# Kernel optimization log

Hardware: AMD Instinct MI355X
Metric: run time of the kernel (lower is better)

The kernel has to match this reference:

```python
import jax, jax.numpy as jnp
import numpy as np

STRIDE = 16
HF = WF = 160
IM_H = IM_W = STRIDE * HF  # 2560
A = 15
PRE_NMS = 3000
RPN_KEEP = 300
RPN_NMS_TH = 0.7
OBJ_TH = 0.2
MIN_SIZE = 8.0
G = 7
OUT_DIM = 10
S = 2  # bilinear samples per bin per axis
NUM_FG = 3
SCORE_TH = 0.3
RCNN_NMS_TH = 0.5
FINAL_KEEP = 100
BBOX_STD = jnp.array([0.1, 0.1, 0.2, 0.2], jnp.float32)


def gen_anchors():
    base = 16.0
    anchors = []
    for r in [0.5, 1.0, 2.0]:
        for s in [2.0, 4.0, 8.0, 16.0, 32.0]:
            size = base * s
            w = size * np.sqrt(1.0 / r)
            h = size * np.sqrt(r)
            anchors.append([-w / 2, -h / 2, w / 2, h / 2])
    return jnp.asarray(np.array(anchors, np.float32))  # [A,4]


def decode_boxes(anchors, deltas):
    d = deltas * BBOX_STD
    wa = anchors[..., 2] - anchors[..., 0] + 1.0
    ha = anchors[..., 3] - anchors[..., 1] + 1.0
    cxa = anchors[..., 0] + 0.5 * wa
    cya = anchors[..., 1] + 0.5 * ha
    cx = d[..., 0] * wa + cxa
    cy = d[..., 1] * ha + cya
    w = wa * jnp.exp(jnp.minimum(d[..., 2], 4.0))
    h = ha * jnp.exp(jnp.minimum(d[..., 3], 4.0))
    boxes = jnp.stack([cx - 0.5 * w, cy - 0.5 * h, cx + 0.5 * w, cy + 0.5 * h], -1)
    hi = jnp.array([IM_W - 1.0, IM_H - 1.0, IM_W - 1.0, IM_H - 1.0], jnp.float32)
    return jnp.clip(boxes, 0.0, hi)


def greedy_nms(boxes, scores, iou_th, keep_n):
    # scores <= 0 means pre-suppressed/invalid
    N = boxes.shape[0]
    areas = jnp.maximum(boxes[:, 2] - boxes[:, 0] + 1.0, 0.0) * jnp.maximum(boxes[:, 3] - boxes[:, 1] + 1.0, 0.0)

    def body(k, st):
        sup, keep = st
        s = jnp.where(sup, -1e30, scores)
        i = jnp.argmax(s)
        valid = s[i] > -1e29
        keep = keep.at[k].set(jnp.where(valid, i.astype(jnp.int32), N))
        bi = boxes[i]
        ix1 = jnp.maximum(bi[0], boxes[:, 0]); iy1 = jnp.maximum(bi[1], boxes[:, 1])
        ix2 = jnp.minimum(bi[2], boxes[:, 2]); iy2 = jnp.minimum(bi[3], boxes[:, 3])
        inter = jnp.maximum(ix2 - ix1 + 1.0, 0.0) * jnp.maximum(iy2 - iy1 + 1.0, 0.0)
        iou = inter / jnp.maximum(areas[i] + areas - inter, 1e-6)
        sup2 = (sup | (iou > iou_th)).at[i].set(True)
        sup = jnp.where(valid, sup2, sup)
        return sup, keep

    sup0 = scores <= 0.0
    keep0 = jnp.full((keep_n,), N, jnp.int32)
    _, keep = jax.lax.fori_loop(0, keep_n, body, (sup0, keep0))
    return keep, keep < N


def rpn_proposal(rpn_cls, rpn_bbox):
    fg = rpn_cls[0, A:]                                           # [A,HF,WF] objectness
    deltas = rpn_bbox[0].reshape(A, 4, HF, WF).transpose(0, 2, 3, 1)  # [A,HF,WF,4]
    anchors = gen_anchors()
    sx = jnp.arange(WF, dtype=jnp.float32) * STRIDE
    sy = jnp.arange(HF, dtype=jnp.float32) * STRIDE
    gx, gy = jnp.meshgrid(sx, sy)                                 # [HF,WF]
    shift = jnp.stack([gx, gy, gx, gy], -1)                       # [HF,WF,4]
    all_anchors = anchors[:, None, None, :] + shift[None]         # [A,HF,WF,4]
    boxes = decode_boxes(all_anchors, deltas).reshape(-1, 4)      # [A*HF*WF,4]
    scores = fg.reshape(-1)
    w = boxes[:, 2] - boxes[:, 0] + 1.0
    h = boxes[:, 3] - boxes[:, 1] + 1.0
    ok = (w >= MIN_SIZE) & (h >= MIN_SIZE) & (scores > OBJ_TH)
    scores = jnp.where(ok, scores, 0.0)
    sc, idx = jax.lax.top_k(scores, PRE_NMS)
    bx = boxes[idx]
    keep, valid = greedy_nms(bx, sc, RPN_NMS_TH, RPN_KEEP)
    bxp = jnp.concatenate([bx, jnp.zeros((1, 4), bx.dtype)], 0)
    rois = bxp[keep] * valid[:, None].astype(bx.dtype)            # [RPN_KEEP,4]
    return rois, valid


def psroi_align(ft, rois, valid):
    # ft [490,HF,WF]; position-sensitive channel = (c*G+ph)*G+pw
    x1 = rois[:, 0] / STRIDE; y1 = rois[:, 1] / STRIDE
    x2 = rois[:, 2] / STRIDE; y2 = rois[:, 3] / STRIDE
    bw = jnp.maximum(x2 - x1, 0.1) / G
    bh = jnp.maximum(y2 - y1, 0.1) / G
    frac = (jnp.arange(S, dtype=jnp.float32) + 0.5) / S           # [S]
    grid = jnp.arange(G, dtype=jnp.float32)[None, :, None] + frac[None, None, :]  # [1,G,S]
    ys = jnp.clip(y1[:, None, None] + grid * bh[:, None, None], 0.0, HF - 1.0)    # [R,G,S]
    xs = jnp.clip(x1[:, None, None] + grid * bw[:, None, None], 0.0, WF - 1.0)
    y0 = jnp.floor(ys); x0 = jnp.floor(xs)
    wy = ys - y0; wx = xs - x0
    y0i = y0.astype(jnp.int32); x0i = x0.astype(jnp.int32)
    y1i = jnp.minimum(y0i + 1, HF - 1); x1i = jnp.minimum(x0i + 1, WF - 1)
    chan = (jnp.arange(OUT_DIM)[:, None, None] * G + jnp.arange(G)[None, :, None]) * G + jnp.arange(G)[None, None, :]
    ch = chan[None, :, :, :, None, None]                          # [1,C,G,G,1,1]
    Y0 = y0i[:, None, :, None, :, None]; Y1 = y1i[:, None, :, None, :, None]
    X0 = x0i[:, None, None, :, None, :]; X1 = x1i[:, None, None, :, None, :]
    WY = wy[:, None, :, None, :, None]; WX = wx[:, None, None, :, None, :]
    v00 = ft[ch, Y0, X0]; v01 = ft[ch, Y0, X1]
    v10 = ft[ch, Y1, X0]; v11 = ft[ch, Y1, X1]                    # [R,C,G,G,S,S]
    val = v00 * (1 - WY) * (1 - WX) + v01 * (1 - WY) * WX + v10 * WY * (1 - WX) + v11 * WY * WX
    pooled = val.mean(axis=(4, 5))                                # [R,C,G,G]
    return pooled * valid[:, None, None, None].astype(pooled.dtype)


def rcnn_proposal(cls_sm, bbox_pred, rois, valid):
    R = rois.shape[0]
    deltas = bbox_pred.reshape(R, 4, 4)[:, 1:, :]                 # [R,3,4] fg classes
    boxes = decode_boxes(rois[:, None, :], deltas)                # [R,3,4]
    scores = cls_sm[:, 1:] * valid[:, None].astype(cls_sm.dtype)  # [R,3]
    scores = jnp.where(scores > SCORE_TH, scores, 0.0)
    fb = boxes.reshape(-1, 4)
    fs = scores.reshape(-1)
    labels = jnp.tile(jnp.arange(1, NUM_FG + 1, dtype=jnp.float32), (R,))
    keep, kv = greedy_nms(fb, fs, RCNN_NMS_TH, FINAL_KEEP)
    fbp = jnp.concatenate([fb, jnp.zeros((1, 4), fb.dtype)], 0)
    fsp = jnp.concatenate([fs, jnp.zeros((1,), fs.dtype)], 0)
    flp = jnp.concatenate([labels, jnp.zeros((1,), labels.dtype)], 0)
    out = jnp.concatenate([fbp[keep], fsp[keep][:, None], flp[keep][:, None]], -1)  # [FINAL_KEEP,6]
    return out * kv[:, None].astype(out.dtype)


def setup_inputs() -> dict:
    key = jax.random.key(0)
    ks = jax.random.split(key, 9)
    return {
        'rpn_cls_prob_reshape': jax.random.uniform(ks[0], (1, 2 * A, HF, WF), jnp.float32),
        'rpn_bbox_pred': jax.random.normal(ks[1], (1, 4 * A, HF, WF), jnp.float32),
        'ft_add_left_right': jax.random.normal(ks[2], (1, OUT_DIM * G * G, HF, WF), jnp.float32),
        'w1': jax.random.normal(ks[3], (490, 2048), jnp.float32) * 0.02,
        'b1': jnp.zeros((2048,), jnp.float32),
        'w_cls': jax.random.normal(ks[4], (2048, 4), jnp.float32) * 0.02,
        'b_cls': jnp.zeros((4,), jnp.float32),
        'w_bbox': jax.random.normal(ks[5], (2048, 16), jnp.float32) * 0.02,
        'b_bbox': jnp.zeros((16,), jnp.float32),
    }


def reference(rpn_cls_prob_reshape, rpn_bbox_pred, ft_add_left_right, w1, b1, w_cls, b_cls, w_bbox, b_bbox):
    rois, valid = rpn_proposal(rpn_cls_prob_reshape, rpn_bbox_pred)
    pooled = psroi_align(ft_add_left_right[0], rois, valid)       # [R,10,7,7]
    feats = pooled.reshape(-1, OUT_DIM * G * G)                   # [R,490]
    h = jax.nn.relu(feats @ w1 + b1)
    cls_sm = jax.nn.softmax(h @ w_cls + b_cls, axis=-1)
    bbox = h @ w_bbox + b_bbox
    return rcnn_proposal(cls_sm, bbox, rois, valid)
```

## Files before the change

kernel.cpp:

```cpp
#include <hip/hip_runtime.h>
#include <stdint.h>

#define HF_ 160
#define WF_ 160
#define HFW 25600
#define A_N 15
#define NTOT 384000
#define PRE_N 3000
#define KEEP_N 300
#define FEAT_N 490
#define HID_N 2048
#define RC_N 900
#define FIN_N 100
#define TIE_CAP 1024
#define NW 47
#define NSTAGE 320
#define RNW 15
#define FC1_MT 10
#define FC1_KP 496
#define ZN (65536 * 2 + 32)

__constant__ float c_hw[15] = {
  22.627416997969522f, 45.254833995939045f, 90.509667991878090f, 181.01933598375618f, 362.03867196751236f,
  16.0f, 32.0f, 64.0f, 128.0f, 256.0f,
  11.313708498984761f, 22.627416997969522f, 45.254833995939045f, 90.509667991878090f, 181.01933598375618f
};
__constant__ float c_hh[15] = {
  11.313708498984761f, 22.627416997969522f, 45.254833995939045f, 90.509667991878090f, 181.01933598375618f,
  16.0f, 32.0f, 64.0f, 128.0f, 256.0f,
  22.627416997969522f, 45.254833995939045f, 90.509667991878090f, 181.01933598375618f, 362.03867196751236f
};

__device__ __forceinline__ void decode_one(
    float ax1, float ay1, float ax2, float ay2,
    float dx, float dy, float dw, float dh,
    float& ox1, float& oy1, float& ox2, float& oy2)
{
#pragma clang fp contract(off)
  float wa = (ax2 - ax1) + 1.0f;
  float ha = (ay2 - ay1) + 1.0f;
  float cxa = ax1 + 0.5f * wa;
  float cya = ay1 + 0.5f * ha;
  float d0 = dx * 0.1f;
  float d1 = dy * 0.1f;
  float d2 = dw * 0.2f;
  float d3 = dh * 0.2f;
  float cx = d0 * wa + cxa;
  float cy = d1 * ha + cya;
  float w  = wa * expf(fminf(d2, 4.0f));
  float h  = ha * expf(fminf(d3, 4.0f));
  float x1 = cx - 0.5f * w;
  float y1 = cy - 0.5f * h;
  float x2 = cx + 0.5f * w;
  float y2 = cy + 0.5f * h;
  ox1 = fminf(fmaxf(x1, 0.0f), 2559.0f);
  oy1 = fminf(fmaxf(y1, 0.0f), 2559.0f);
  ox2 = fminf(fmaxf(x2, 0.0f), 2559.0f);
  oy2 = fminf(fmaxf(y2, 0.0f), 2559.0f);
}

__device__ __forceinline__ float iou_ref(
    float ax1, float ay1, float ax2, float ay2, float areaA,
    float bx1, float by1, float bx2, float by2)
{
#pragma clang fp contract(off)
  float ix1 = fmaxf(ax1, bx1);
  float iy1 = fmaxf(ay1, by1);
  float ix2 = fminf(ax2, bx2);
  float iy2 = fminf(ay2, by2);
  float iw = fmaxf((ix2 - ix1) + 1.0f, 0.0f);
  float ih = fmaxf((iy2 - iy1) + 1.0f, 0.0f);
  float inter = iw * ih;
  float areaB = fmaxf((bx2 - bx1) + 1.0f, 0.0f) * fmaxf((by2 - by1) + 1.0f, 0.0f);
  float den = fmaxf(areaA + areaB - inter, 1e-6f);
  return inter / den;
}

__global__ void k_decode_score(const float* __restrict__ cls,
                               const float* __restrict__ bbox,
                               float* __restrict__ scores,
                               uint32_t* __restrict__ histzero)
{
  int e = blockIdx.x * 256 + threadIdx.x;
  if (e < ZN) histzero[e] = 0u;
  if (e >= NTOT) return;
  int a   = e / HFW;
  int rem = e - a * HFW;
  int i   = rem / WF_;
  int j   = rem - i * WF_;
  float score = cls[(A_N + a) * HFW + rem];
  float gx = (float)(j * 16);
  float gy = (float)(i * 16);
  float hw = c_hw[a], hh = c_hh[a];
  float dx = bbox[(a * 4 + 0) * HFW + rem];
  float dy = bbox[(a * 4 + 1) * HFW + rem];
  float dw = bbox[(a * 4 + 2) * HFW + rem];
  float dh = bbox[(a * 4 + 3) * HFW + rem];
  float x1, y1, x2, y2;
  decode_one(gx - hw, gy - hh, gx + hw, gy + hh, dx, dy, dw, dh, x1, y1, x2, y2);
  float bw, bh;
  {
#pragma clang fp contract(off)
    bw = (x2 - x1) + 1.0f;
    bh = (y2 - y1) + 1.0f;
  }
  bool ok = (bw >= 8.0f) && (bh >= 8.0f) && (score > 0.2f);
  scores[e] = ok ? score : 0.0f;
}

__global__ void k_hist_hi(const float* __restrict__ scores, uint32_t* __restrict__ hist)
{
  __shared__ uint32_t lh[512];
  int t = threadIdx.x;
  for (int i = t; i < 512; i += 256) lh[i] = 0u;
  __syncthreads();
  int e = blockIdx.x * 256 + t;
  if (e < NTOT) {
    float s = scores[e];
    if (s > 0.0f) {
      uint32_t b = __float_as_uint(s) >> 16;
      if (b >= 0x3E00u && b < 0x4000u) atomicAdd(&lh[b - 0x3E00u], 1u);
      else atomicAdd(&hist[b], 1u);
    }
  }
  __syncthreads();
  for (int i = t; i < 512; i += 256) {
    uint32_t v = lh[i];
    if (v) atomicAdd(&hist[0x3E00u + i], v);
  }
}

__global__ void __launch_bounds__(1024) k_findbin1(const uint32_t* __restrict__ hist,
                                                   uint32_t* __restrict__ meta)
{
  __shared__ uint32_t sfx[1024];
  __shared__ int s_chunk;
  __shared__ uint32_t s_exc;
  int t = threadIdx.x;
  if (t == 0) s_chunk = -1;
  const uint32_t* hp = hist + t * 64;
  uint32_t s = 0;
#pragma unroll
  for (int b = 0; b < 64; b++) s += hp[b];
  sfx[t] = s;
  __syncthreads();
  for (int d = 1; d < 1024; d <<= 1) {
    uint32_t v = (t + d < 1024) ? sfx[t + d] : 0u;
    __syncthreads();
    sfx[t] += v;
    __syncthreads();
  }
  uint32_t inc = sfx[t];
  uint32_t exc = (t < 1023) ? sfx[t + 1] : 0u;
  if (exc < (uint32_t)PRE_N && inc >= (uint32_t)PRE_N) { s_chunk = t; s_exc = exc; }
  __syncthreads();
  int c = s_chunk;
  if (c < 0) {
    if (t == 0) { meta[0] = 0u; meta[1] = 0u; meta[2] = 1u; }
    return;
  }
  if (t < 64) {
    uint32_t h = hist[c * 64 + t];
    uint32_t v = h;
#pragma unroll
    for (int d = 1; d < 64; d <<= 1) {
      uint32_t o = (uint32_t)__shfl_down((int)v, d);
      v += (t + d < 64) ? o : 0u;
    }
    uint32_t before = s_exc + (v - h);
    if (before < (uint32_t)PRE_N && before + h >= (uint32_t)PRE_N) {
      meta[0] = (uint32_t)(c * 64 + t);
      meta[1] = (uint32_t)PRE_N - before;
      meta[2] = 0u;
    }
  }
}

__global__ void k_hist_lo(const float* __restrict__ scores,
                          const uint32_t* __restrict__ meta,
                          uint32_t* __restrict__ hist2)
{
  if (meta[2]) return;
  uint32_t B1 = meta[0];
  int e = blockIdx.x * 256 + threadIdx.x;
  if (e >= NTOT) return;
  float s = scores[e];
  if (s <= 0.0f) return;
  uint32_t bits = __float_as_uint(s);
  if ((bits >> 16) == B1) atomicAdd(&hist2[bits & 0xFFFFu], 1u);
}

__global__ void __launch_bounds__(1024) k_findT(const uint32_t* __restrict__ hist2,
                                                uint32_t* __restrict__ meta)
{
  if (meta[2]) { if (threadIdx.x == 0) meta[3] = 0u; return; }
  __shared__ uint32_t sfx[1024];
  __shared__ int s_chunk;
  __shared__ uint32_t s_exc;
  int t = threadIdx.x;
  if (t == 0) s_chunk = -1;
  uint32_t K = meta[1];
  const uint32_t* hp = hist2 + t * 64;
  uint32_t s = 0;
#pragma unroll
  for (int b = 0; b < 64; b++) s += hp[b];
  sfx[t] = s;
  __syncthreads();
  for (int d = 1; d < 1024; d <<= 1) {
    uint32_t v = (t + d < 1024) ? sfx[t + d] : 0u;
    __syncthreads();
    sfx[t] += v;
    __syncthreads();
  }
  uint32_t inc = sfx[t];
  uint32_t exc = (t < 1023) ? sfx[t + 1] : 0u;
  if (exc < K && inc >= K) { s_chunk = t; s_exc = exc; }
  __syncthreads();
  int c = s_chunk;
  if (c < 0) { if (t == 0) meta[3] = 0u; return; }
  if (t < 64) {
    uint32_t h = hist2[c * 64 + t];
    uint32_t v = h;
#pragma unroll
    for (int d = 1; d < 64; d <<= 1) {
      uint32_t o = (uint32_t)__shfl_down((int)v, d);
      v += (t + d < 64) ? o : 0u;
    }
    uint32_t before = s_exc + (v - h);
    if (before < K && before + h >= K)
      meta[3] = (meta[0] << 16) | (uint32_t)(c * 64 + t);
  }
}

__global__ void k_compact(const float* __restrict__ scores,
                          const uint32_t* __restrict__ meta,
                          uint64_t* __restrict__ gt,
                          uint64_t* __restrict__ tie,
                          uint32_t* __restrict__ cnts)
{
  int e = blockIdx.x * 256 + threadIdx.x;
  if (e >= NTOT) return;
  float s = scores[e];
  if (s <= 0.0f) return;
  uint32_t bits = __float_as_uint(s);
  uint32_t T = meta[3];
  uint64_t key = ((uint64_t)bits << 32) | (uint32_t)(~(uint32_t)e);
  if (bits > T) {
    uint32_t p = atomicAdd(&cnts[0], 1u);
    if (p < (uint32_t)PRE_N) gt[p] = key;
  } else if (bits == T) {
    uint32_t p = atomicAdd(&cnts[1], 1u);
    if (p < (uint32_t)TIE_CAP) tie[p] = key;
  }
}

__global__ void __launch_bounds__(1024) k_sort_gather(
    const uint64_t* __restrict__ gt,
    const uint64_t* __restrict__ tie,
    const uint32_t* __restrict__ cnts,
    const float* __restrict__ bbox,
    float* __restrict__ bxx1, float* __restrict__ bxy1,
    float* __restrict__ bxx2, float* __restrict__ bxy2)
{
  __shared__ uint64_t key[4096];
  int t = threadIdx.x;
  uint32_t ngt = min(cnts[0], (uint32_t)PRE_N);
  uint32_t nte = min(cnts[1], (uint32_t)TIE_CAP);
  for (int s = t; s < 4096; s += 1024) {
    uint64_t k = 0;
    if ((uint32_t)s < ngt) k = gt[s];
    else if ((uint32_t)s < ngt + nte) k = tie[s - ngt];
    key[s] = k;
  }
  for (unsigned size = 2; size <= 4096; size <<= 1) {
    for (unsigned stride = size >> 1; stride > 0; stride >>= 1) {
      __syncthreads();
      for (unsigned i = t; i < 4096; i += 1024) {
        unsigned p = i ^ stride;
        if (p > i) {
          bool desc = ((i & size) == 0);
          uint64_t a = key[i], b = key[p];
          if (desc ? (a < b) : (a > b)) { key[i] = b; key[p] = a; }
        }
      }
    }
  }
  __syncthreads();
  for (int s = t; s < PRE_N; s += 1024) {
    uint64_t k = key[s];
    int idx = (int)(~(uint32_t)(k & 0xFFFFFFFFull));
    float x1 = 0.f, y1 = 0.f, x2 = 0.f, y2 = 0.f;
    if (idx >= 0) {
      int a   = idx / HFW;
      int rem = idx - a * HFW;
      int i   = rem / WF_;
      int j   = rem - i * WF_;
      float gx = (float)(j * 16);
      float gy = (float)(i * 16);
      float hw = c_hw[a], hh = c_hh[a];
      float dx = bbox[(a * 4 + 0) * HFW + rem];
      float dy = bbox[(a * 4 + 1) * HFW + rem];
      float dw = bbox[(a * 4 + 2) * HFW + rem];
      float dh = bbox[(a * 4 + 3) * HFW + rem];
      decode_one(gx - hw, gy - hh, gx + hw, gy + hh, dx, dy, dw, dh, x1, y1, x2, y2);
    }
    bxx1[s] = x1; bxy1[s] = y1; bxx2[s] = x2; bxy2[s] = y2;
  }
}

__global__ void __launch_bounds__(256) k_iou_mask(
    const float* __restrict__ bxx1, const float* __restrict__ bxy1,
    const float* __restrict__ bxx2, const float* __restrict__ bxy2,
    uint64_t* __restrict__ rowmask, uint64_t* __restrict__ diag)
{
  __shared__ float s1[PRE_N], s2[PRE_N], s3[PRE_N], s4[PRE_N];
  int t = threadIdx.x;
  for (int e = t; e < PRE_N; e += 256) {
    s1[e] = bxx1[e]; s2[e] = bxy1[e]; s3[e] = bxx2[e]; s4[e] = bxy2[e];
  }
  __syncthreads();
  int task = blockIdx.x * 256 + t;
  if (task >= PRE_N * NW) return;
  int row = task / NW;
  int w   = task - row * NW;
  if ((w + 1) * 64 <= row) {
    rowmask[(size_t)row * NW + w] = 0;
    return;
  }
  float ax1 = s1[row], ay1 = s2[row], ax2 = s3[row], ay2 = s4[row];
  float areaA;
  {
#pragma clang fp contract(off)
    areaA = fmaxf((ax2 - ax1) + 1.0f, 0.0f) * fmaxf((ay2 - ay1) + 1.0f, 0.0f);
  }
  int j0 = w << 6;
  uint64_t bits = 0;
  for (int off = 0; off < 64; off++) {
    int jj = (off + t) & 63;
    int j = j0 + jj;
    if (j < PRE_N) {
      float iou = iou_ref(ax1, ay1, ax2, ay2, areaA, s1[j], s2[j], s3[j], s4[j]);
      if (iou > 0.7f) bits |= 1ull << jj;
    }
  }
  rowmask[(size_t)row * NW + w] = bits;
  if (w == (row >> 6)) diag[row] = bits;
}

__global__ void __launch_bounds__(256) k_rpn_scan(
    const float* __restrict__ bxx1, const float* __restrict__ bxy1,
    const float* __restrict__ bxx2, const float* __restrict__ bxy2,
    const uint32_t* __restrict__ cnts,
    const uint64_t* __restrict__ rowmask,
    const uint64_t* __restrict__ diag,
    float* __restrict__ rois, uint32_t* __restrict__ valid)
{
  __shared__ uint64_t rowstage[NSTAGE * NW];
  __shared__ uint64_t sdiag[PRE_N];
  __shared__ int keepIdx[KEEP_N];
  __shared__ int s_nkeep;
  int t = threadIdx.x;
  for (int e = t; e < NSTAGE * NW; e += 256) rowstage[e] = rowmask[e];
  for (int e = t; e < PRE_N; e += 256) sdiag[e] = diag[e];
  __syncthreads();
  if (t < 64) {
    int lane = t;
    uint32_t Mp = min(cnts[0] + min(cnts[1], (uint32_t)TIE_CAP), (uint32_t)PRE_N);
    uint64_t sup = 0, pend = 0;
    int nk = 0;
    int nwords = (int)((Mp + 63u) >> 6);
    for (int w = 0; w < nwords && nk < KEEP_N; w++) {
      sup |= pend; pend = 0;
      uint64_t cw = (uint64_t)__shfl((unsigned long long)sup, w);
      int lim = (int)Mp - (w << 6);
      uint64_t range = (lim >= 64) ? ~0ull : ((1ull << lim) - 1ull);
      uint64_t rem = (~cw) & range;
      while (rem && nk < KEEP_N) {
        int b = __builtin_ctzll(rem);
        int i = (w << 6) + b;
        if (lane == 0) keepIdx[nk] = i;
        nk++;
        uint64_t roww = sdiag[i];
        uint64_t rowl = 0;
        if (lane < NW)
          rowl = (i < NSTAGE) ? rowstage[i * NW + lane]
                              : rowmask[(size_t)i * NW + lane];
        sup |= pend;
        pend = rowl;
        rem &= ~(roww | (1ull << b));
      }
    }
    sup |= pend;
    if (lane == 0) s_nkeep = nk;
  }
  __syncthreads();
  int nk2 = s_nkeep;
  for (int k = t; k < nk2; k += 256) {
    int i = keepIdx[k];
    rois[k * 4 + 0] = bxx1[i];
    rois[k * 4 + 1] = bxy1[i];
    rois[k * 4 + 2] = bxx2[i];
    rois[k * 4 + 3] = bxy2[i];
    valid[k] = 1u;
  }
  for (int e = nk2 * 4 + t; e < KEEP_N * 4; e += 256) rois[e] = 0.0f;
  for (int e = nk2 + t; e < KEEP_N; e += 256) valid[e] = 0u;
}

__global__ void __launch_bounds__(512) k_psroi(const float* __restrict__ ft,
                                               const float* __restrict__ rois,
                                               const uint32_t* __restrict__ valid,
                                               float* __restrict__ feats)
{
#pragma clang fp contract(off)
  int r = blockIdx.x;
  int t = threadIdx.x;
  if (t >= FEAT_N) return;
  float x1 = rois[r * 4 + 0] * 0.0625f;
  float y1 = rois[r * 4 + 1] * 0.0625f;
  float x2 = rois[r * 4 + 2] * 0.0625f;
  float y2 = rois[r * 4 + 3] * 0.0625f;
  float bw = fmaxf(x2 - x1, 0.1f) / 7.0f;
  float bh = fmaxf(y2 - y1, 0.1f) / 7.0f;
  int c   = t / 49;
  int rem = t - c * 49;
  int gy  = rem / 7;
  int gx  = rem - gy * 7;
  (void)c;
  const float* base = ft + t * HFW;
  float acc = 0.0f;
  for (int sy = 0; sy < 2; sy++) {
    float gyf = (float)gy + (sy ? 0.75f : 0.25f);
    float ys = fminf(fmaxf(y1 + gyf * bh, 0.0f), 159.0f);
    float y0f = floorf(ys);
    float wy = ys - y0f;
    int y0 = (int)y0f;
    int y1i = min(y0 + 1, 159);
    for (int sx = 0; sx < 2; sx++) {
      float gxf = (float)gx + (sx ? 0.75f : 0.25f);
      float xs = fminf(fmaxf(x1 + gxf * bw, 0.0f), 159.0f);
      float x0f = floorf(xs);
      float wx = xs - x0f;
      int x0 = (int)x0f;
      int x1i = min(x0 + 1, 159);
      float v00 = base[y0 * WF_ + x0];
      float v01 = base[y0 * WF_ + x1i];
      float v10 = base[y1i * WF_ + x0];
      float v11 = base[y1i * WF_ + x1i];
      float val = v00 * (1.0f - wy) * (1.0f - wx)
                + v01 * (1.0f - wy) * wx
                + v10 * wy * (1.0f - wx)
                + v11 * wy * wx;
      acc += val;
    }
  }
  float pooled = acc * 0.25f;
  feats[r * FEAT_N + t] = valid[r] ? pooled : 0.0f;
}

__global__ void __launch_bounds__(256) k_fc1(const float* __restrict__ feats,
                                             const float* __restrict__ w1,
                                             const float* __restrict__ b1,
                                             float* __restrict__ h)
{
  __shared__ float sf[FC1_MT][FC1_KP];
  int t = threadIdx.x;
  int n = blockIdx.x * 256 + t;
  int m0 = blockIdx.y * FC1_MT;
  for (int idx = t; idx < FC1_MT * FC1_KP; idx += 256) {
    int mm = idx / FC1_KP;
    int kk = idx - mm * FC1_KP;
    sf[mm][kk] = (kk < FEAT_N) ? feats[(m0 + mm) * FEAT_N + kk] : 0.0f;
  }
  __syncthreads();
  float acc[FC1_MT];
#pragma unroll
  for (int i = 0; i < FC1_MT; i++) acc[i] = 0.0f;
  float wb[16];
#pragma unroll
  for (int u = 0; u < 16; u++) wb[u] = w1[u * HID_N + n];
#pragma unroll 1
  for (int kb = 0; kb < FC1_KP - 16; kb += 16) {
    float wn[16];
    int kn = kb + 16;
#pragma unroll
    for (int u = 0; u < 16; u++)
      wn[u] = (kn + u < FEAT_N) ? w1[(kn + u) * HID_N + n] : 0.0f;
#pragma unroll
    for (int u4 = 0; u4 < 4; u4++) {
#pragma unroll
      for (int i = 0; i < FC1_MT; i++) {
        float4 f = *reinterpret_cast<const float4*>(&sf[i][kb + u4 * 4]);
        acc[i] = fmaf(f.x, wb[u4 * 4 + 0], acc[i]);
        acc[i] = fmaf(f.y, wb[u4 * 4 + 1], acc[i]);
        acc[i] = fmaf(f.z, wb[u4 * 4 + 2], acc[i]);
        acc[i] = fmaf(f.w, wb[u4 * 4 + 3], acc[i]);
      }
    }
#pragma unroll
    for (int u = 0; u < 16; u++) wb[u] = wn[u];
  }
  {
    const int kb = FC1_KP - 16;
#pragma unroll
    for (int u4 = 0; u4 < 4; u4++) {
#pragma unroll
      for (int i = 0; i < FC1_MT; i++) {
        float4 f = *reinterpret_cast<const float4*>(&sf[i][kb + u4 * 4]);
        acc[i] = fmaf(f.x, wb[u4 * 4 + 0], acc[i]);
        acc[i] = fmaf(f.y, wb[u4 * 4 + 1], acc[i]);
        acc[i] = fmaf(f.z, wb[u4 * 4 + 2], acc[i]);
        acc[i] = fmaf(f.w, wb[u4 * 4 + 3], acc[i]);
      }
    }
  }
  float b = b1[n];
#pragma unroll
  for (int i = 0; i < FC1_MT; i++) h[(m0 + i) * HID_N + n] = fmaxf(acc[i] + b, 0.0f);
}

__global__ void __launch_bounds__(256) k_fc2(const float* __restrict__ h,
                                             const float* __restrict__ w_cls,
                                             const float* __restrict__ b_cls,
                                             const float* __restrict__ w_bbox,
                                             const float* __restrict__ b_bbox,
                                             const uint32_t* __restrict__ valid,
                                             float* __restrict__ scores3,
                                             float* __restrict__ bbox16)
{
  int r = blockIdx.x;
  int t = threadIdx.x;
  float acc[20];
#pragma unroll
  for (int i = 0; i < 20; i++) acc[i] = 0.0f;
  for (int k = t; k < HID_N; k += 256) {
    float hv = h[r * HID_N + k];
    float4 wc = *reinterpret_cast<const float4*>(w_cls + k * 4);
    acc[0] = fmaf(hv, wc.x, acc[0]);
    acc[1] = fmaf(hv, wc.y, acc[1]);
    acc[2] = fmaf(hv, wc.z, acc[2]);
    acc[3] = fmaf(hv, wc.w, acc[3]);
#pragma unroll
    for (int q = 0; q < 4; q++) {
      float4 wb = *reinterpret_cast<const float4*>(w_bbox + k * 16 + q * 4);
      acc[4 + q * 4 + 0] = fmaf(hv, wb.x, acc[4 + q * 4 + 0]);
      acc[4 + q * 4 + 1] = fmaf(hv, wb.y, acc[4 + q * 4 + 1]);
      acc[4 + q * 4 + 2] = fmaf(hv, wb.z, acc[4 + q * 4 + 2]);
      acc[4 + q * 4 + 3] = fmaf(hv, wb.w, acc[4 + q * 4 + 3]);
    }
  }
#pragma unroll
  for (int off = 32; off > 0; off >>= 1) {
#pragma unroll
    for (int i = 0; i < 20; i++) acc[i] += __shfl_down(acc[i], off);
  }
  __shared__ float red[4][20];
  int wid = t >> 6, lane = t & 63;
  if (lane == 0) {
#pragma unroll
    for (int i = 0; i < 20; i++) red[wid][i] = acc[i];
  }
  __syncthreads();
  if (t == 0) {
    float f[20];
#pragma unroll
    for (int i = 0; i < 20; i++) f[i] = red[0][i] + red[1][i] + red[2][i] + red[3][i];
    float l0 = f[0] + b_cls[0];
    float l1 = f[1] + b_cls[1];
    float l2 = f[2] + b_cls[2];
    float l3 = f[3] + b_cls[3];
    float m = fmaxf(fmaxf(l0, l1), fmaxf(l2, l3));
    float e0 = expf(l0 - m), e1 = expf(l1 - m), e2 = expf(l2 - m), e3 = expf(l3 - m);
    float s = ((e0 + e1) + e2) + e3;
    float vf = valid[r] ? 1.0f : 0.0f;
    scores3[r * 3 + 0] = (e1 / s) * vf;
    scores3[r * 3 + 1] = (e2 / s) * vf;
    scores3[r * 3 + 2] = (e3 / s) * vf;
#pragma unroll
    for (int i = 0; i < 16; i++) bbox16[r * 16 + i] = f[4 + i] + b_bbox[i];
  }
}

__global__ void __launch_bounds__(1024) k_rc_sortdec(
    const float* __restrict__ rois,
    const float* __restrict__ scores3,
    const float* __restrict__ bbox16,
    float* __restrict__ sx1, float* __restrict__ sy1,
    float* __restrict__ sx2, float* __restrict__ sy2,
    float* __restrict__ ssc, int* __restrict__ sidx,
    uint32_t* __restrict__ rc_meta)
{
  __shared__ uint64_t key[1024];
  __shared__ float bx[RC_N], by[RC_N], bX[RC_N], bY[RC_N];
  int t = threadIdx.x;
  uint64_t k = 0;
  if (t < RC_N) {
    int r = t / 3;
    int c = t - r * 3;
    float ax1 = rois[r * 4 + 0], ay1 = rois[r * 4 + 1];
    float ax2 = rois[r * 4 + 2], ay2 = rois[r * 4 + 3];
    int cb = (c + 1) * 4;
    float dx = bbox16[r * 16 + cb + 0];
    float dy = bbox16[r * 16 + cb + 1];
    float dw = bbox16[r * 16 + cb + 2];
    float dh = bbox16[r * 16 + cb + 3];
    float x1, y1, x2, y2;
    decode_one(ax1, ay1, ax2, ay2, dx, dy, dw, dh, x1, y1, x2, y2);
    bx[t] = x1; by[t] = y1; bX[t] = x2; bY[t] = y2;
    float sc = scores3[t];
    if (sc > 0.3f)
      k = ((uint64_t)__float_as_uint(sc) << 32) | (uint32_t)(~(uint32_t)t);
  }
  key[t] = k;
  for (unsigned size = 2; size <= 1024; size <<= 1) {
    for (unsigned stride = size >> 1; stride > 0; stride >>= 1) {
      __syncthreads();
      unsigned p = t ^ stride;
      if (p > (unsigned)t) {
        bool desc = ((t & size) == 0);
        uint64_t a = key[t], b = key[p];
        if (desc ? (a < b) : (a > b)) { key[t] = b; key[p] = a; }
      }
    }
  }
  __syncthreads();
  uint64_t kk = key[t];
  if ((kk == 0) && (t == 0 || key[t - 1] != 0)) rc_meta[0] = (uint32_t)t;
  if (t < RC_N) {
    int m = (int)(~(uint32_t)(kk & 0xFFFFFFFFull));
    sidx[t] = m;
    ssc[t] = __uint_as_float((uint32_t)(kk >> 32));
    float a = 0.f, b = 0.f, c = 0.f, d = 0.f;
    if (m >= 0) { a = bx[m]; b = by[m]; c = bX[m]; d = bY[m]; }
    sx1[t] = a; sy1[t] = b; sx2[t] = c; sy2[t] = d;
  }
}

__global__ void __launch_bounds__(256) k_rc_mask(
    const float* __restrict__ sx1, const float* __restrict__ sy1,
    const float* __restrict__ sx2, const float* __restrict__ sy2,
    uint64_t* __restrict__ rcmask, uint64_t* __restrict__ rcdiag)
{
  __shared__ float s1[RC_N], s2[RC_N], s3[RC_N], s4[RC_N];
  int t = threadIdx.x;
  for (int e = t; e < RC_N; e += 256) {
    s1[e] = sx1[e]; s2[e] = sy1[e]; s3[e] = sx2[e]; s4[e] = sy2[e];
  }
  __syncthreads();
  int task = blockIdx.x * 256 + t;
  if (task >= RC_N * RNW) return;
  int row = task / RNW;
  int w   = task - row * RNW;
  if ((w + 1) * 64 <= row) {
    rcmask[(size_t)row * RNW + w] = 0;
    return;
  }
  float ax1 = s1[row], ay1 = s2[row], ax2 = s3[row], ay2 = s4[row];
  float areaA;
  {
#pragma clang fp contract(off)
    areaA = fmaxf((ax2 - ax1) + 1.0f, 0.0f) * fmaxf((ay2 - ay1) + 1.0f, 0.0f);
  }
  int j0 = w << 6;
  uint64_t bits = 0;
  for (int off = 0; off < 64; off++) {
    int jj = (off + t) & 63;
    int j = j0 + jj;
    if (j < RC_N) {
      float iou = iou_ref(ax1, ay1, ax2, ay2, areaA, s1[j], s2[j], s3[j], s4[j]);
      if (iou > 0.5f) bits |= 1ull << jj;
    }
  }
  rcmask[(size_t)row * RNW + w] = bits;
  if (w == (row >> 6)) rcdiag[row] = bits;
}

__global__ void __launch_bounds__(256) k_rc_scan(
    const float* __restrict__ sx1, const float* __restrict__ sy1,
    const float* __restrict__ sx2, const float* __restrict__ sy2,
    const float* __restrict__ ssc, const int* __restrict__ sidx,
    const uint32_t* __restrict__ rc_meta,
    const uint64_t* __restrict__ rcmask,
    const uint64_t* __restrict__ rcdiag,
    float* __restrict__ out)
{
  __shared__ uint64_t rowstage[RC_N * RNW];
  __shared__ uint64_t sdiag[RC_N];
  __shared__ int keepPos[FIN_N];
  __shared__ int s_nk;
  int t = threadIdx.x;
  for (int e = t; e < RC_N * RNW; e += 256) rowstage[e] = rcmask[e];
  for (int e = t; e < RC_N; e += 256) sdiag[e] = rcdiag[e];
  __syncthreads();
  if (t < 64) {
    int lane = t;
    int Npos = (int)min(rc_meta[0], (uint32_t)RC_N);
    uint64_t sup = 0, pend = 0;
    int nk = 0;
    int nwords = (Npos + 63) >> 6;
    for (int w = 0; w < nwords && nk < FIN_N; w++) {
      sup |= pend; pend = 0;
      uint64_t cw = (uint64_t)__shfl((unsigned long long)sup, w);
      int lim = Npos - (w << 6);
      uint64_t range = (lim >= 64) ? ~0ull : ((1ull << lim) - 1ull);
      uint64_t rem = (~cw) & range;
      while (rem && nk < FIN_N) {
        int b = __builtin_ctzll(rem);
        int i = (w << 6) + b;
        if (lane == 0) keepPos[nk] = i;
        nk++;
        uint64_t roww = sdiag[i];
        uint64_t rowl = (lane < RNW) ? rowstage[i * RNW + lane] : 0;
        sup |= pend;
        pend = rowl;
        rem &= ~(roww | (1ull << b));
      }
    }
    sup |= pend;
    if (lane == 0) s_nk = nk;
  }
  __syncthreads();
  int nk = s_nk;
  for (int k = t; k < nk; k += 256) {
    int i = keepPos[k];
    int m = sidx[i];
    out[k * 6 + 0] = sx1[i];
    out[k * 6 + 1] = sy1[i];
    out[k * 6 + 2] = sx2[i];
    out[k * 6 + 3] = sy2[i];
    out[k * 6 + 4] = ssc[i];
    out[k * 6 + 5] = (float)(m - (m / 3) * 3 + 1);
  }
  for (int e = nk * 6 + t; e < FIN_N * 6; e += 256) out[e] = 0.0f;
}

extern "C" void kernel_launch(void* const* d_in, const int* in_sizes, int n_in,
                              void* d_out, int out_size, void* d_ws, size_t ws_size,
                              hipStream_t stream)
{
  (void)in_sizes; (void)n_in; (void)out_size; (void)ws_size;
  const float* rpn_cls  = (const float*)d_in[0];
  const float* rpn_bbox = (const float*)d_in[1];
  const float* ft       = (const float*)d_in[2];
  const float* w1       = (const float*)d_in[3];
  const float* b1       = (const float*)d_in[4];
  const float* w_cls    = (const float*)d_in[5];
  const float* b_cls    = (const float*)d_in[6];
  const float* w_bbox   = (const float*)d_in[7];
  const float* b_bbox   = (const float*)d_in[8];
  float* out = (float*)d_out;

  char* ws = (char*)d_ws;
  size_t off = 0;
  auto alloc = [&](size_t bytes) -> void* {
    void* p = (void*)(ws + off);
    off += (bytes + 15) & ~(size_t)15;
    return p;
  };
  uint32_t* hist1  = (uint32_t*)alloc(65536 * 4);
  uint32_t* hist2  = (uint32_t*)alloc(65536 * 4);
  uint32_t* meta   = (uint32_t*)alloc(32 * 4);
  float*    scores = (float*)alloc((size_t)NTOT * 4);
  uint64_t* gt     = (uint64_t*)alloc(3008 * 8);
  uint64_t* tie    = (uint64_t*)alloc(TIE_CAP * 8);
  float*    bxx1 = (float*)alloc(PRE_N * 4);
  float*    bxy1 = (float*)alloc(PRE_N * 4);
  float*    bxx2 = (float*)alloc(PRE_N * 4);
  float*    bxy2 = (float*)alloc(PRE_N * 4);
  float*    rois  = (float*)alloc(KEEP_N * 4 * 4);
  uint32_t* valid = (uint32_t*)alloc(KEEP_N * 4);
  float*    feats = (float*)alloc((size_t)KEEP_N * FEAT_N * 4);
  float*    hbuf  = (float*)alloc((size_t)KEEP_N * HID_N * 4);
  float*    scores3 = (float*)alloc(RC_N * 4);
  float*    bbox16  = (float*)alloc(KEEP_N * 16 * 4);
  float*    sx1 = (float*)alloc(RC_N * 4);
  float*    sy1 = (float*)alloc(RC_N * 4);
  float*    sx2 = (float*)alloc(RC_N * 4);
  float*    sy2 = (float*)alloc(RC_N * 4);
  float*    ssc = (float*)alloc(RC_N * 4);
  int*      sidx = (int*)alloc(RC_N * 4);
  uint32_t* rc_meta = (uint32_t*)alloc(16 * 4);
  uint64_t* rowmask = (uint64_t*)alloc((size_t)3008 * NW * 8);
  uint64_t* diag    = (uint64_t*)alloc(3008 * 8);
  uint64_t* rcmask  = (uint64_t*)alloc((size_t)RC_N * RNW * 8);
  uint64_t* rcdiag  = (uint64_t*)alloc(904 * 8);

  k_decode_score<<<NTOT / 256, 256, 0, stream>>>(rpn_cls, rpn_bbox, scores, hist1);
  k_hist_hi<<<NTOT / 256, 256, 0, stream>>>(scores, hist1);
  k_findbin1<<<1, 1024, 0, stream>>>(hist1, meta);
  k_hist_lo<<<NTOT / 256, 256, 0, stream>>>(scores, meta, hist2);
  k_findT<<<1, 1024, 0, stream>>>(hist2, meta);
  k_compact<<<NTOT / 256, 256, 0, stream>>>(scores, meta, gt, tie, meta + 8);
  k_sort_gather<<<1, 1024, 0, stream>>>(gt, tie, meta + 8, rpn_bbox,
                                        bxx1, bxy1, bxx2, bxy2);
  k_iou_mask<<<(PRE_N * NW + 255) / 256, 256, 0, stream>>>(bxx1, bxy1, bxx2, bxy2,
                                                           rowmask, diag);
  k_rpn_scan<<<1, 256, 0, stream>>>(bxx1, bxy1, bxx2, bxy2, meta + 8,
                                    rowmask, diag, rois, valid);
  k_psroi<<<KEEP_N, 512, 0, stream>>>(ft, rois, valid, feats);
  k_fc1<<<dim3(HID_N / 256, KEEP_N / FC1_MT), 256, 0, stream>>>(feats, w1, b1, hbuf);
  k_fc2<<<KEEP_N, 256, 0, stream>>>(hbuf, w_cls, b_cls, w_bbox, b_bbox, valid,
                                    scores3, bbox16);
  k_rc_sortdec<<<1, 1024, 0, stream>>>(rois, scores3, bbox16,
                                       sx1, sy1, sx2, sy2, ssc, sidx, rc_meta);
  k_rc_mask<<<(RC_N * RNW + 255) / 256, 256, 0, stream>>>(sx1, sy1, sx2, sy2,
                                                          rcmask, rcdiag);
  k_rc_scan<<<1, 256, 0, stream>>>(sx1, sy1, sx2, sy2, ssc, sidx, rc_meta,
                                   rcmask, rcdiag, out);
}
```

Before: 470.4 us.

## Replace bitonic sorts with parallel rank-by-counting scatter in both NMS stages

Both single-block bitonic sorts are replaced by rank counting. Each valid key counts how many keys in shared memory are larger, then writes its decoded box directly to that rank slot. The RPN stage now runs across 16 blocks of 256 threads instead of one 1024-thread block. This removes the many barrier-separated compare-exchange stages and the shared-memory gather buffers. The cost is quadratic comparisons, mostly broadcast shared-memory reads. Output slots past the valid count are no longer zero-filled, so downstream kernels must honour the count.

```diff
diff --git a/kernel.cpp b/kernel.cpp
--- a/kernel.cpp
+++ b/kernel.cpp
@@ -254,7 +254,7 @@
   }
 }
 
-__global__ void __launch_bounds__(1024) k_sort_gather(
+__global__ void __launch_bounds__(256) k_rank_gather(
     const uint64_t* __restrict__ gt,
     const uint64_t* __restrict__ tie,
     const uint32_t* __restrict__ cnts,
@@ -262,50 +262,49 @@
     float* __restrict__ bxx1, float* __restrict__ bxy1,
     float* __restrict__ bxx2, float* __restrict__ bxy2)
 {
-  __shared__ uint64_t key[4096];
+  __shared__ uint64_t keys[4096];
   int t = threadIdx.x;
   uint32_t ngt = min(cnts[0], (uint32_t)PRE_N);
   uint32_t nte = min(cnts[1], (uint32_t)TIE_CAP);
-  for (int s = t; s < 4096; s += 1024) {
+  uint32_t M = ngt + nte;
+  for (int s = t; s < 4096; s += 256) {
     uint64_t k = 0;
     if ((uint32_t)s < ngt) k = gt[s];
-    else if ((uint32_t)s < ngt + nte) k = tie[s - ngt];
-    key[s] = k;
-  }
-  for (unsigned size = 2; size <= 4096; size <<= 1) {
-    for (unsigned stride = size >> 1; stride > 0; stride >>= 1) {
-      __syncthreads();
-      for (unsigned i = t; i < 4096; i += 1024) {
-        unsigned p = i ^ stride;
-        if (p > i) {
-          bool desc = ((i & size) == 0);
-          uint64_t a = key[i], b = key[p];
-          if (desc ? (a < b) : (a > b)) { key[i] = b; key[p] = a; }
-        }
-      }
-    }
-  }
-  __syncthreads();
-  for (int s = t; s < PRE_N; s += 1024) {
-    uint64_t k = key[s];
-    int idx = (int)(~(uint32_t)(k & 0xFFFFFFFFull));
-    float x1 = 0.f, y1 = 0.f, x2 = 0.f, y2 = 0.f;
-    if (idx >= 0) {
-      int a   = idx / HFW;
-      int rem = idx - a * HFW;
-      int i   = rem / WF_;
-      int j   = rem - i * WF_;
-      float gx = (float)(j * 16);
-      float gy = (float)(i * 16);
-      float hw = c_hw[a], hh = c_hh[a];
-      float dx = bbox[(a * 4 + 0) * HFW + rem];
-      float dy = bbox[(a * 4 + 1) * HFW + rem];
-      float dw = bbox[(a * 4 + 2) * HFW + rem];
-      float dh = bbox[(a * 4 + 3) * HFW + rem];
-      decode_one(gx - hw, gy - hh, gx + hw, gy + hh, dx, dy, dw, dh, x1, y1, x2, y2);
-    }
-    bxx1[s] = x1; bxy1[s] = y1; bxx2[s] = x2; bxy2[s] = y2;
-  }
+    else if ((uint32_t)s < M) k = tie[s - ngt];
+    keys[s] = k;
+  }
+  __syncthreads();
+  int e = blockIdx.x * 256 + t;
+  uint64_t my = keys[e];
+  if (my == 0) return;
+  int r = 0;
+#pragma unroll 4
+  for (int j = 0; j < 4096; j += 4) {
+    uint64_t k0 = keys[j + 0];
+    uint64_t k1 = keys[j + 1];
+    uint64_t k2 = keys[j + 2];
+    uint64_t k3 = keys[j + 3];
+    r += (k0 > my) ? 1 : 0;
+    r += (k1 > my) ? 1 : 0;
+    r += (k2 > my) ? 1 : 0;
+    r += (k3 > my) ? 1 : 0;
+  }
+  if (r >= PRE_N) return;
+  int idx = (int)(~(uint32_t)(my & 0xFFFFFFFFull));
+  int a   = idx / HFW;
+  int rem = idx - a * HFW;
+  int i   = rem / WF_;
+  int j   = rem - i * WF_;
+  float gx = (float)(j * 16);
+  float gy = (float)(i * 16);
+  float hw = c_hw[a], hh = c_hh[a];
+  float dx = bbox[(a * 4 + 0) * HFW + rem];
+  float dy = bbox[(a * 4 + 1) * HFW + rem];
+  float dw = bbox[(a * 4 + 2) * HFW + rem];
+  float dh = bbox[(a * 4 + 3) * HFW + rem];
+  float x1, y1, x2, y2;
+  decode_one(gx - hw, gy - hh, gx + hw, gy + hh, dx, dy, dw, dh, x1, y1, x2, y2);
+  bxx1[r] = x1; bxy1[r] = y1; bxx2[r] = x2; bxy2[r] = y2;
 }
 
 __global__ void __launch_bounds__(256) k_iou_mask(
@@ -581,7 +580,7 @@
   }
 }
 
-__global__ void __launch_bounds__(1024) k_rc_sortdec(
+__global__ void __launch_bounds__(1024) k_rc_rank(
     const float* __restrict__ rois,
     const float* __restrict__ scores3,
     const float* __restrict__ bbox16,
@@ -590,10 +589,12 @@
     float* __restrict__ ssc, int* __restrict__ sidx,
     uint32_t* __restrict__ rc_meta)
 {
-  __shared__ uint64_t key[1024];
-  __shared__ float bx[RC_N], by[RC_N], bX[RC_N], bY[RC_N];
-  int t = threadIdx.x;
+  __shared__ uint64_t keys[1024];
+  __shared__ int s_npos;
+  int t = threadIdx.x;
+  if (t == 0) s_npos = 0;
   uint64_t k = 0;
+  float x1 = 0.f, y1 = 0.f, x2 = 0.f, y2 = 0.f, sc = 0.f;
   if (t < RC_N) {
     int r = t / 3;
     int c = t - r * 3;
@@ -604,36 +605,30 @@
     float dy = bbox16[r * 16 + cb + 1];
     float dw = bbox16[r * 16 + cb + 2];
     float dh = bbox16[r * 16 + cb + 3];
-    float x1, y1, x2, y2;
     decode_one(ax1, ay1, ax2, ay2, dx, dy, dw, dh, x1, y1, x2, y2);
-    bx[t] = x1; by[t] = y1; bX[t] = x2; bY[t] = y2;
-    float sc = scores3[t];
+    sc = scores3[t];
     if (sc > 0.3f)
       k = ((uint64_t)__float_as_uint(sc) << 32) | (uint32_t)(~(uint32_t)t);
   }
-  key[t] = k;
-  for (unsigned size = 2; size <= 1024; size <<= 1) {
-    for (unsigned stride = size >> 1; stride > 0; stride >>= 1) {
-      __syncthreads();
-      unsigned p = t ^ stride;
-      if (p > (unsigned)t) {
-        bool desc = ((t & size) == 0);
-        uint64_t a = key[t], b = key[p];
-        if (desc ? (a < b) : (a > b)) { key[t] = b; key[p] = a; }
-      }
-    }
-  }
-  __syncthreads();
-  uint64_t kk = key[t];
-  if ((kk == 0) && (t == 0 || key[t - 1] != 0)) rc_meta[0] = (uint32_t)t;
-  if (t < RC_N) {
-    int m = (int)(~(uint32_t)(kk & 0xFFFFFFFFull));
-    sidx[t] = m;
-    ssc[t] = __uint_as_float((uint32_t)(kk >> 32));
-    float a = 0.f, b = 0.f, c = 0.f, d = 0.f;
-    if (m >= 0) { a = bx[m]; b = by[m]; c = bX[m]; d = bY[m]; }
-    sx1[t] = a; sy1[t] = b; sx2[t] = c; sy2[t] = d;
-  }
+  keys[t] = k;
+  if (k != 0) atomicAdd(&s_npos, 1);
+  __syncthreads();
+  if (t == 0) rc_meta[0] = (uint32_t)s_npos;
+  if (k == 0) return;
+  int r = 0;
+#pragma unroll 4
+  for (int j = 0; j < 1024; j += 4) {
+    uint64_t k0 = keys[j + 0];
+    uint64_t k1 = keys[j + 1];
+    uint64_t k2 = keys[j + 2];
+    uint64_t k3 = keys[j + 3];
+    r += (k0 > k) ? 1 : 0;
+    r += (k1 > k) ? 1 : 0;
+    r += (k2 > k) ? 1 : 0;
+    r += (k3 > k) ? 1 : 0;
+  }
+  sx1[r] = x1; sy1[r] = y1; sx2[r] = x2; sy2[r] = y2;
+  ssc[r] = sc; sidx[r] = t;
 }
 
 __global__ void __launch_bounds__(256) k_rc_mask(
@@ -791,7 +786,7 @@
   k_hist_lo<<<NTOT / 256, 256, 0, stream>>>(scores, meta, hist2);
   k_findT<<<1, 1024, 0, stream>>>(hist2, meta);
   k_compact<<<NTOT / 256, 256, 0, stream>>>(scores, meta, gt, tie, meta + 8);
-  k_sort_gather<<<1, 1024, 0, stream>>>(gt, tie, meta + 8, rpn_bbox,
+  k_rank_gather<<<16, 256, 0, stream>>>(gt, tie, meta + 8, rpn_bbox,
                                         bxx1, bxy1, bxx2, bxy2);
   k_iou_mask<<<(PRE_N * NW + 255) / 256, 256, 0, stream>>>(bxx1, bxy1, bxx2, bxy2,
                                                            rowmask, diag);
@@ -801,8 +796,8 @@
   k_fc1<<<dim3(HID_N / 256, KEEP_N / FC1_MT), 256, 0, stream>>>(feats, w1, b1, hbuf);
   k_fc2<<<KEEP_N, 256, 0, stream>>>(hbuf, w_cls, b_cls, w_bbox, b_bbox, valid,
                                     scores3, bbox16);
-  k_rc_sortdec<<<1, 1024, 0, stream>>>(rois, scores3, bbox16,
-                                       sx1, sy1, sx2, sy2, ssc, sidx, rc_meta);
+  k_rc_rank<<<1, 1024, 0, stream>>>(rois, scores3, bbox16,
+                                    sx1, sy1, sx2, sy2, ssc, sidx, rc_meta);
   k_rc_mask<<<(RC_N * RNW + 255) / 256, 256, 0, stream>>>(sx1, sy1, sx2, sy2,
                                                           rcmask, rcdiag);
   k_rc_scan<<<1, 256, 0, stream>>>(sx1, sy1, sx2, sy2, ssc, sidx, rc_meta,
```

Result: no change. 470.6 us (+0.0%).
